# Kernel optimization log

Measured on AMD Instinct MI355X. Metric: run time of the kernel, lower is better.

## Reference

```python
import jax, jax.numpy as jnp
import numpy as np

NTYPES = 2
B, N, MNEI = 4, 512, 100
M = MNEI * NTYPES          # neighbor slots = maxNeighborNum * ntypes
EMB_LAST = 100             # embedding net sizes [25, 50, 100]
FIT_H = 240
M2 = 16
RMIN, RMAX = 0.5, 6.0


def setup_inputs():
    key = jax.random.key(0)
    ks = jax.random.split(key, 24)
    r = jax.random.uniform(ks[0], (B, N, M), minval=0.6, maxval=7.0)
    v = jax.random.normal(ks[1], (B, N, M, 3))
    v = v / jnp.linalg.norm(v, axis=-1, keepdims=True)
    keep = jax.random.uniform(ks[2], (B, N, M)) < 0.7
    ImageDR = jnp.concatenate([r[..., None], r[..., None] * v], axis=-1)
    ImageDR = jnp.where(keep[..., None], ImageDR, 0.0).astype(jnp.float32)
    Imagetype_map = jax.random.randint(ks[3], (N,), 0, NTYPES)
    list_neigh = jax.random.randint(ks[4], (B, N, M), 0, N + 1)
    type_map = jnp.arange(NTYPES)
    davg = (0.01 * jax.random.normal(ks[5], (NTYPES, M, 4))).astype(jnp.float32)
    dstd = (1.0 + 0.1 * jax.random.uniform(ks[6], (NTYPES, M, 4))).astype(jnp.float32)

    def w(k, shape, fan):
        return (jax.random.normal(k, shape) / np.sqrt(fan)).astype(jnp.float32)

    def b(k, shape):
        return (0.1 * jax.random.normal(k, shape)).astype(jnp.float32)

    emb_W0 = w(ks[7], (NTYPES, NTYPES, 1, 25), 1)
    emb_b0 = b(ks[8], (NTYPES, NTYPES, 25))
    emb_W1 = w(ks[9], (NTYPES, NTYPES, 25, 50), 25)
    emb_b1 = b(ks[10], (NTYPES, NTYPES, 50))
    emb_W2 = w(ks[11], (NTYPES, NTYPES, 50, 100), 50)
    emb_b2 = b(ks[12], (NTYPES, NTYPES, 100))
    fin = M2 * EMB_LAST
    fit_W0 = w(ks[13], (NTYPES, fin, FIT_H), fin)
    fit_b0 = b(ks[14], (NTYPES, FIT_H))
    fit_W1 = w(ks[15], (NTYPES, FIT_H, FIT_H), FIT_H)
    fit_b1 = b(ks[16], (NTYPES, FIT_H))
    fit_W2 = w(ks[17], (NTYPES, FIT_H, FIT_H), FIT_H)
    fit_b2 = b(ks[18], (NTYPES, FIT_H))
    fit_W3 = w(ks[19], (NTYPES, FIT_H, 1), FIT_H)
    fit_b3 = b(ks[20], (NTYPES, 1))
    energy_shift = jnp.array([-3.37, -5.21], dtype=jnp.float32)
    return dict(list_neigh=list_neigh, Imagetype_map=Imagetype_map, type_map=type_map,
                ImageDR=ImageDR, nghost=0, davg=davg, dstd=dstd,
                emb_W0=emb_W0, emb_b0=emb_b0, emb_W1=emb_W1, emb_b1=emb_b1,
                emb_W2=emb_W2, emb_b2=emb_b2,
                fit_W0=fit_W0, fit_b0=fit_b0, fit_W1=fit_W1, fit_b1=fit_b1,
                fit_W2=fit_W2, fit_b2=fit_b2, fit_W3=fit_W3, fit_b3=fit_b3,
                energy_shift=energy_shift)


def _emb(s, W0, b0, W1, b1, W2, b2):
    # DeepPot-SE embedding net with doubling resnet connections
    h = jnp.tanh(s @ W0 + b0)                                   # [..., 25]
    h = jnp.tanh(h @ W1 + b1) + jnp.concatenate([h, h], -1)     # [..., 50]
    return jnp.tanh(h @ W2 + b2) + jnp.concatenate([h, h], -1)  # [..., 100]


def _fit(d, W0, b0, W1, b1, W2, b2, W3, b3):
    h = jnp.tanh(d @ W0 + b0)
    h = h + jnp.tanh(h @ W1 + b1)
    h = h + jnp.tanh(h @ W2 + b2)
    return h @ W3 + b3


def _forward(ImageDR, davg, dstd,
             emb_W0, emb_b0, emb_W1, emb_b1, emb_W2, emb_b2,
             fit_W0, fit_b0, fit_W1, fit_b1, fit_W2, fit_b2, fit_W3, fit_b3,
             energy_shift, Imagetype_map):
    Bsz, Nat, Mtot, _ = ImageDR.shape
    m = Mtot // NTYPES
    R = ImageDR[..., 0]
    Rsafe = jnp.where(R > 1e-5, R, 1.0)
    # smooth switching function s(r): 1/r below Rmin, polynomial taper to Rmax
    u = (R - RMIN) / (RMAX - RMIN)
    mid = (u ** 3 * (-6.0 * u * u + 15.0 * u - 10.0) + 1.0) / Rsafe
    S = jnp.where((R > 0) & (R < RMIN), 1.0 / Rsafe,
                  jnp.where((R > RMIN) & (R < RMAX), mid, 0.0))
    msk = (jnp.abs(R) > 1e-5)[..., None]
    Ri = jnp.concatenate([S[..., None],
                          jnp.where(msk, (S / Rsafe)[..., None] * ImageDR[..., 1:4], 0.0)],
                         axis=-1)                                    # [B,N,M,4] = (s, s*x/r, s*y/r, s*z/r)
    # per-center-type normalization (irregular gather of stats)
    Rn = (Ri - davg[Imagetype_map][None]) / dstd[Imagetype_map][None]
    tmask = [(Imagetype_map == i).astype(Rn.dtype)[None, :, None, None] for i in range(NTYPES)]
    xyz = jnp.zeros((Bsz, Nat, 4, EMB_LAST), Rn.dtype)
    for j in range(NTYPES):                                          # neighbor-type slice
        sl = Rn[:, :, j * m:(j + 1) * m, :]                          # [B,N,m,4]
        s = sl[..., 0:1]
        G = jnp.zeros(sl.shape[:3] + (EMB_LAST,), sl.dtype)
        for i in range(NTYPES):                                      # center type -> pair net (i, j)
            G = G + tmask[i] * _emb(s, emb_W0[i, j], emb_b0[i, j],
                                    emb_W1[i, j], emb_b1[i, j], emb_W2[i, j], emb_b2[i, j])
        xyz = xyz + jnp.einsum('bnmk,bnmc->bnkc', sl, G)
    xyz = xyz / (m * NTYPES)
    # descriptor D = (Ri^T G)^T (Ri^T G)[:, :M2], flattened -> [B,N,EMB_LAST*M2]
    D = jnp.einsum('bnkc,bnkd->bncd', xyz, xyz[..., :M2]).reshape(Bsz, Nat, -1)
    Ei = jnp.zeros((Bsz, Nat), D.dtype)
    for i in range(NTYPES):
        e = _fit(D, fit_W0[i], fit_b0[i], fit_W1[i], fit_b1[i],
                 fit_W2[i], fit_b2[i], fit_W3[i], fit_b3[i])[..., 0] + energy_shift[i]
        Ei = Ei + tmask[i][:, :, 0, 0] * e
    Etot = jnp.sum(Ei, axis=1)
    return Etot, Ei


def reference(list_neigh, Imagetype_map, type_map, ImageDR, nghost, davg, dstd,
              emb_W0, emb_b0, emb_W1, emb_b1, emb_W2, emb_b2,
              fit_W0, fit_b0, fit_W1, fit_b1, fit_W2, fit_b2, fit_W3, fit_b3,
              energy_shift):
    return _forward(ImageDR, davg, dstd,
                    emb_W0, emb_b0, emb_W1, emb_b1, emb_W2, emb_b2,
                    fit_W0, fit_b0, fit_W1, fit_b1, fit_W2, fit_b2, fit_W3, fit_b3,
                    energy_shift, Imagetype_map)
```

## Files before the change

### kernel.cpp

```cpp
#include <hip/hip_runtime.h>
#include <math.h>

#define NT 2
#define BSZ 4
#define NAT 512
#define NATOMS 2048
#define NNEI 200
#define EMB 100
#define FITH 240
#define DDIM 1600
#define TBK 1024

#define USH_BYTE 6208
#define TBL_U   0
#define W0T_U   409600
#define W1T_U   (W0T_U + 819200)
#define W2T_U   (W1T_U + 262144)
#define D_U     (W2T_U + 262144)
#define H0_U    (D_U + 3276800)
#define USH_END (H0_U + 1048576)
#define WS_NEED ((size_t)USH_BYTE + (size_t)USH_END * 2)

typedef short s8v __attribute__((ext_vector_type(8)));
typedef float f16v __attribute__((ext_vector_type(16)));

__device__ __forceinline__ float ftanh(float x) {
    float ax = fabsf(x);
    float e = __expf(2.0f * ax);
    float t = 1.0f - __fdividef(2.0f, e + 1.0f);
    return (x < 0.0f) ? -t : t;
}
__device__ __forceinline__ unsigned short f2bf(float f) {
    unsigned u = __float_as_uint(f);
    u += 0x7FFFu + ((u >> 16) & 1u);
    return (unsigned short)(u >> 16);
}
__device__ __forceinline__ float bf2f(unsigned short s) {
    return __uint_as_float(((unsigned)s) << 16);
}
__device__ __forceinline__ float calc_S(float R) {
    float Rsafe = (R > 1e-5f) ? R : 1.0f;
    float u = (R - 0.5f) * (1.0f / 5.5f);
    float uu = u * u;
    float mid = (u * uu * (-6.0f * uu + 15.0f * u - 10.0f) + 1.0f) / Rsafe;
    float S = 0.0f;
    if (R > 0.0f && R < 0.5f)      S = 1.0f / Rsafe;
    else if (R > 0.5f && R < 6.0f) S = mid;
    return S;
}

#define N_W0 819200
#define N_W1 262144
#define N_W2 262144
#define N_B  1536
__global__ void wtrans_kernel(const float* __restrict__ fW0, const float* __restrict__ fW1,
                              const float* __restrict__ fW2,
                              const float* __restrict__ fb0, const float* __restrict__ fb1,
                              const float* __restrict__ fb2,
                              float* __restrict__ ws, float* __restrict__ out) {
    if (blockIdx.x == 0 && threadIdx.x < 4) out[threadIdx.x] = 0.0f;
    unsigned short* u0 = (unsigned short*)((char*)ws + USH_BYTE);
    int id = blockIdx.x * 256 + threadIdx.x;
    if (id < N_W0) {
        int k = id / 512, n = id - k * 512;
        float v = 0.0f;
        if (n < 240)                 v = fW0[(size_t)k * 240 + n];
        else if (n >= 256 && n < 496) v = fW0[(size_t)(1600 + k) * 240 + (n - 256)];
        u0[W0T_U + (size_t)n * 1600 + k] = f2bf(v);
        return;
    }
    id -= N_W0;
    if (id < N_W1) {
        int k = id / 512, n = id - k * 512;
        float v = 0.0f;
        if (n < 240 && k < 240)      v = fW1[(size_t)k * 240 + n];
        else if (n >= 256 && n < 496 && k >= 256 && k < 496)
                                     v = fW1[(size_t)(240 + (k - 256)) * 240 + (n - 256)];
        u0[W1T_U + (size_t)n * 512 + k] = f2bf(v);
        return;
    }
    id -= N_W1;
    if (id < N_W2) {
        int k = id / 512, n = id - k * 512;
        float v = 0.0f;
        if (n < 240 && k < 240)      v = fW2[(size_t)k * 240 + n];
        else if (n >= 256 && n < 496 && k >= 256 && k < 496)
                                     v = fW2[(size_t)(240 + (k - 256)) * 240 + (n - 256)];
        u0[W2T_U + (size_t)n * 512 + k] = f2bf(v);
        return;
    }
    id -= N_W2;
    if (id < N_B) {
        int l = id / 512, n = id - l * 512;
        const float* fb = (l == 0) ? fb0 : (l == 1) ? fb1 : fb2;
        float v = 0.0f;
        if (n < 240)                 v = fb[n];
        else if (n >= 256 && n < 496) v = fb[240 + (n - 256)];
        ws[16 + l * 512 + n] = v;
    }
}

__global__ void __launch_bounds__(256) table_kernel(
    const float* __restrict__ davg, const float* __restrict__ dstd,
    const float* __restrict__ eW0, const float* __restrict__ eb0,
    const float* __restrict__ eW1, const float* __restrict__ eb1,
    const float* __restrict__ eW2, const float* __restrict__ eb2,
    float* __restrict__ ws)
{
    __shared__ float los[100], his[100];
    __shared__ float rng[2];
    __shared__ float h0s[8][25];
    __shared__ float h1s[8][50];
    const int bx = blockIdx.x;
    const int nid = bx >> 7;
    const int kb  = (bx & 127) * 8;
    const int t = nid >> 1, j = nid & 1;
    const int tid = threadIdx.x;

    if (tid < 100) {
        int m = j * 100 + tid;
        float av = davg[(t * NNEI + m) * 4];
        float sd = dstd[(t * NNEI + m) * 4];
        float inv = __fdividef(1.0f, sd);
        float a = (0.0f - av) * inv;
        float b = (2.0f - av) * inv;
        los[tid] = fminf(a, b);
        his[tid] = fmaxf(a, b);
    }
    __syncthreads();
    if (tid == 0) {
        float lo = los[0], hi = his[0];
        for (int i = 1; i < 100; ++i) { lo = fminf(lo, los[i]); hi = fmaxf(hi, his[i]); }
        rng[0] = lo; rng[1] = hi - lo;
        if (kb == 0) {
            ws[nid * 2] = lo;
            ws[nid * 2 + 1] = (float)(TBK - 1) / (hi - lo);
        }
    }
    __syncthreads();
    const float smin = rng[0], span = rng[1];
    const float* W0 = eW0 + nid * 25;
    const float* B0 = eb0 + nid * 25;
    if (tid < 200) {
        int q = tid / 25, a = tid % 25;
        float s = smin + span * ((float)(kb + q) * (1.0f / (TBK - 1)));
        h0s[q][a] = ftanh(fmaf(s, W0[a], B0[a]));
    }
    __syncthreads();
    const float* W1 = eW1 + nid * 1250;
    const float* B1 = eb1 + nid * 50;
    for (int idx = tid; idx < 400; idx += 256) {
        int q = idx / 50, cc = idx % 50;
        float acc = B1[cc];
#pragma unroll
        for (int a = 0; a < 25; ++a) acc = fmaf(h0s[q][a], W1[a * 50 + cc], acc);
        h1s[q][cc] = ftanh(acc) + h0s[q][(cc < 25) ? cc : cc - 25];
    }
    __syncthreads();
    const float* W2 = eW2 + nid * 5000;
    const float* B2 = eb2 + nid * 100;
    unsigned short* tblu = (unsigned short*)((char*)ws + USH_BYTE) + TBL_U;
    for (int idx = tid; idx < 800; idx += 256) {
        int q = idx / 100, c = idx % 100;
        float acc = B2[c];
#pragma unroll
        for (int a = 0; a < 50; ++a) acc = fmaf(h1s[q][a], W2[a * 100 + c], acc);
        float g = ftanh(acc) + h1s[q][(c < 50) ? c : c - 50];
        tblu[(size_t)(nid * TBK + kb + q) * 100 + c] = f2bf(g);
    }
}

__global__ void __launch_bounds__(128) embed_kernel(
    const int* __restrict__ itype, const float* __restrict__ imagedr,
    const float* __restrict__ davg, const float* __restrict__ dstd,
    float* __restrict__ ws)
{
    __shared__ __align__(16) float4 srn[NNEI];
    __shared__ float sx[NNEI];
    __shared__ float part[2][400];
    const int atom = blockIdx.x;
    const int n = atom & (NAT - 1);
    const int tid = threadIdx.x;
    const int t = itype[n];
    unsigned short* u0 = (unsigned short*)((char*)ws + USH_BYTE);

    const float sm0 = ws[(t * 2 + 0) * 2], sc0 = ws[(t * 2 + 0) * 2 + 1];
    const float sm1 = ws[(t * 2 + 1) * 2], sc1 = ws[(t * 2 + 1) * 2 + 1];

    for (int m = tid; m < NNEI; m += 128) {
        float4 dr = ((const float4*)imagedr)[(size_t)atom * NNEI + m];
        float R = dr.x;
        float S = calc_S(R);
        float Rsafe = (R > 1e-5f) ? R : 1.0f;
        float sr = (fabsf(R) > 1e-5f) ? (S / Rsafe) : 0.0f;
        float4 av = ((const float4*)davg)[t * NNEI + m];
        float4 sd = ((const float4*)dstd)[t * NNEI + m];
        float4 rv;
        rv.x = (S         - av.x) / sd.x;
        rv.y = (sr * dr.y - av.y) / sd.y;
        rv.z = (sr * dr.z - av.z) / sd.z;
        rv.w = (sr * dr.w - av.w) / sd.w;
        srn[m] = rv;
        float smin = (m >= 100) ? sm1 : sm0;
        float scal = (m >= 100) ? sc1 : sc0;
        sx[m] = fminf(fmaxf((rv.x - smin) * scal, 0.0f), (float)(TBK - 2) + 0.9999f);
    }
    __syncthreads();

    const int w = tid >> 6, lane = tid & 63;
    const unsigned short* T = u0 + TBL_U + (size_t)(t * 2 + w) * TBK * EMB;
    const bool hi = (lane < 36);
    float xA0 = 0, xA1 = 0, xA2 = 0, xA3 = 0;
    float xB0 = 0, xB1 = 0, xB2 = 0, xB3 = 0;
    for (int mi = 0; mi < 100; ++mi) {
        int m = w * 100 + mi;
        float4 rv = srn[m];
        float x = sx[m];
        int i = (int)x;
        float f = x - (float)i;
        const unsigned short* Tr = T + (size_t)i * EMB;
        float g0 = bf2f(Tr[lane]);
        float g1 = bf2f(Tr[EMB + lane]);
        float g = fmaf(f, g1 - g0, g0);
        xA0 = fmaf(rv.x, g, xA0); xA1 = fmaf(rv.y, g, xA1);
        xA2 = fmaf(rv.z, g, xA2); xA3 = fmaf(rv.w, g, xA3);
        if (hi) {
            float h0v = bf2f(Tr[64 + lane]);
            float h1v = bf2f(Tr[EMB + 64 + lane]);
            float g2 = fmaf(f, h1v - h0v, h0v);
            xB0 = fmaf(rv.x, g2, xB0); xB1 = fmaf(rv.y, g2, xB1);
            xB2 = fmaf(rv.z, g2, xB2); xB3 = fmaf(rv.w, g2, xB3);
        }
    }
    part[w][0 * 100 + lane] = xA0; part[w][1 * 100 + lane] = xA1;
    part[w][2 * 100 + lane] = xA2; part[w][3 * 100 + lane] = xA3;
    if (hi) {
        part[w][0 * 100 + 64 + lane] = xB0; part[w][1 * 100 + 64 + lane] = xB1;
        part[w][2 * 100 + 64 + lane] = xB2; part[w][3 * 100 + 64 + lane] = xB3;
    }
    __syncthreads();
    const float inv = 1.0f / 200.0f;
    for (int idx = tid; idx < 400; idx += 128)
        part[0][idx] = (part[0][idx] + part[1][idx]) * inv;
    __syncthreads();
    unsigned short* Drow = u0 + D_U + (size_t)atom * DDIM;
    const float* xt = part[0];
    for (int idx = tid; idx < DDIM; idx += 128) {
        int c = idx >> 4, d = idx & 15;
        float s = xt[c] * xt[d] + xt[100 + c] * xt[100 + d]
                + xt[200 + c] * xt[200 + d] + xt[300 + c] * xt[300 + d];
        Drow[idx] = f2bf(s);
    }
}

__global__ void __launch_bounds__(256) gemm_kernel(
    const unsigned short* __restrict__ A, int lda,
    const unsigned short* __restrict__ BT, int ldb,
    const float* __restrict__ bias,
    const unsigned short* __restrict__ Res,
    unsigned short* __restrict__ Out, int ldo,
    int ksteps, int diag)
{
    __shared__ unsigned short Al[64][40];
    __shared__ unsigned short Bl[64][40];
    const int nt = blockIdx.x;
    const int mt = blockIdx.y;
    const int tid = threadIdx.x;
    const int w = tid >> 6, lane = tid & 63;
    const int wm = (w >> 1) * 32, wn = (w & 1) * 32;
    const int m0 = mt * 64, n0 = nt * 64;
    const int k_start = (diag && nt >= 4) ? 256 : 0;
    const int r4 = tid >> 2, c8 = (tid & 3) * 8;

    f16v acc;
#pragma unroll
    for (int i = 0; i < 16; ++i) acc[i] = 0.0f;

    for (int kt = 0; kt < ksteps; ++kt) {
        const int kc = k_start + kt * 32 + c8;
        uint4 av = *(const uint4*)(A  + (size_t)(m0 + r4) * lda + kc);
        uint4 bv = *(const uint4*)(BT + (size_t)(n0 + r4) * ldb + kc);
        __syncthreads();
        *(uint4*)&Al[r4][c8] = av;
        *(uint4*)&Bl[r4][c8] = bv;
        __syncthreads();
        const int fr = (lane >> 5) * 8;
        s8v a0 = *(const s8v*)&Al[wm + (lane & 31)][fr];
        s8v b0 = *(const s8v*)&Bl[wn + (lane & 31)][fr];
        acc = __builtin_amdgcn_mfma_f32_32x32x16_bf16(a0, b0, acc, 0, 0, 0);
        s8v a1 = *(const s8v*)&Al[wm + (lane & 31)][16 + fr];
        s8v b1 = *(const s8v*)&Bl[wn + (lane & 31)][16 + fr];
        acc = __builtin_amdgcn_mfma_f32_32x32x16_bf16(a1, b1, acc, 0, 0, 0);
    }

    const int gcol = n0 + wn + (lane & 31);
    const float bv = bias[gcol];
#pragma unroll
    for (int r = 0; r < 16; ++r) {
        int row = (r & 3) + 8 * (r >> 2) + 4 * (lane >> 5);
        size_t gi = (size_t)(m0 + wm + row) * ldo + gcol;
        float v = ftanh(acc[r] + bv);
        if (Res) v += bf2f(Res[gi]);
        Out[gi] = f2bf(v);
    }
}

__global__ void __launch_bounds__(256) final_kernel(
    const int* __restrict__ itype, const float* ws,
    const float* __restrict__ fW3, const float* __restrict__ fb3,
    const float* __restrict__ eshift, float* __restrict__ out)
{
    __shared__ float sred[4];
    const int tid = threadIdx.x;
    const int w = tid >> 6, lane = tid & 63;
    const int atom = blockIdx.x * 4 + w;
    const int n = atom & (NAT - 1);
    const int t = itype[n];
    const unsigned short* H = (const unsigned short*)((const char*)ws + USH_BYTE) + H0_U;
    const unsigned short* Hrow = H + (size_t)atom * 512 + t * 256;
    float p = 0.0f;
    if (lane < 60) {
        ushort4 hv = *(const ushort4*)(Hrow + lane * 4);
        const float* w3p = fW3 + t * 240 + lane * 4;
        p = bf2f(hv.x) * w3p[0] + bf2f(hv.y) * w3p[1]
          + bf2f(hv.z) * w3p[2] + bf2f(hv.w) * w3p[3];
    }
#pragma unroll
    for (int off = 32; off > 0; off >>= 1) p += __shfl_down(p, off, 64);
    if (lane == 0) {
        float e = p + fb3[t] + eshift[t];
        out[4 + atom] = e;
        sred[w] = e;
    }
    __syncthreads();
    if (tid == 0) {
        int b = (blockIdx.x * 4) >> 9;
        atomicAdd(&out[b], sred[0] + sred[1] + sred[2] + sred[3]);
    }
}

__global__ void dp_atom_kernel(
    const int* __restrict__ itype, const float* __restrict__ imagedr,
    const float* __restrict__ davg, const float* __restrict__ dstd,
    const float* __restrict__ eW0, const float* __restrict__ eb0,
    const float* __restrict__ eW1, const float* __restrict__ eb1,
    const float* __restrict__ eW2, const float* __restrict__ eb2,
    const float* __restrict__ fW0, const float* __restrict__ fb0,
    const float* __restrict__ fW1, const float* __restrict__ fb1,
    const float* __restrict__ fW2, const float* __restrict__ fb2,
    const float* __restrict__ fW3, const float* __restrict__ fb3,
    const float* __restrict__ eshift, float* __restrict__ out)
{
    __shared__ __align__(16) float4 rn4[NNEI];
    __shared__ __align__(16) float  xyz[4 * EMB];
    __shared__ __align__(16) float  h0s[100 * 25];
    __shared__ __align__(16) float  smem[100 * 52];
    const int atom = blockIdx.x;
    const int n = atom & (NAT - 1);
    const int tid = threadIdx.x;
    const int t = itype[n];
    for (int m = tid; m < NNEI; m += 256) {
        float4 dr = ((const float4*)imagedr)[(size_t)atom * NNEI + m];
        float R = dr.x;
        float S = calc_S(R);
        float Rsafe = (R > 1e-5f) ? R : 1.0f;
        float sr = (fabsf(R) > 1e-5f) ? (S / Rsafe) : 0.0f;
        float4 av = ((const float4*)davg)[t * NNEI + m];
        float4 sd = ((const float4*)dstd)[t * NNEI + m];
        float4 rv;
        rv.x = (S - av.x) / sd.x; rv.y = (sr * dr.y - av.y) / sd.y;
        rv.z = (sr * dr.z - av.z) / sd.z; rv.w = (sr * dr.w - av.w) / sd.w;
        rn4[m] = rv;
    }
    const int c = tid & 127; const int mh = tid >> 7;
    float xp0 = 0, xp1 = 0, xp2 = 0, xp3 = 0;
    for (int j = 0; j < NT; ++j) {
        const int wb = t * NT + j;
        const float* W0 = eW0 + wb * 25; const float* B0 = eb0 + wb * 25;
        const float* W1 = eW1 + wb * 1250; const float* B1 = eb1 + wb * 50;
        const float* W2 = eW2 + wb * 5000; const float* B2 = eb2 + wb * 100;
        __syncthreads();
        for (int idx = tid; idx < 2500; idx += 256) {
            int m = idx / 25, a = idx - m * 25;
            h0s[idx] = ftanh(fmaf(rn4[j * 100 + m].x, W0[a], B0[a]));
        }
        __syncthreads();
        for (int idx = tid; idx < 5000; idx += 256) {
            int m = idx / 50, cc = idx - m * 50;
            const float* h0m = h0s + m * 25;
            float acc = B1[cc];
#pragma unroll
            for (int a = 0; a < 25; ++a) acc = fmaf(h0m[a], W1[a * 50 + cc], acc);
            smem[m * 52 + cc] = ftanh(acc) + h0m[(cc < 25) ? cc : cc - 25];
        }
        for (int idx = tid; idx < 200; idx += 256)
            smem[(idx >> 1) * 52 + 50 + (idx & 1)] = 0.0f;
        __syncthreads();
        if (c < EMB) {
            float w2c[52];
#pragma unroll
            for (int a = 0; a < 50; ++a) w2c[a] = W2[a * EMB + c];
            w2c[50] = 0; w2c[51] = 0;
            const float bc = B2[c];
            const int sk = (c < 50) ? c : c - 50;
            for (int i = 0; i < 50; ++i) {
                int m = mh * 50 + i;
                const float* h1m = smem + m * 52;
                float acc = bc;
#pragma unroll
                for (int q = 0; q < 13; ++q) {
                    float4 hv = ((const float4*)h1m)[q];
                    acc = fmaf(hv.x, w2c[4 * q], acc); acc = fmaf(hv.y, w2c[4 * q + 1], acc);
                    acc = fmaf(hv.z, w2c[4 * q + 2], acc); acc = fmaf(hv.w, w2c[4 * q + 3], acc);
                }
                float g = ftanh(acc) + h1m[sk];
                float4 rm = rn4[j * 100 + m];
                xp0 = fmaf(rm.x, g, xp0); xp1 = fmaf(rm.y, g, xp1);
                xp2 = fmaf(rm.z, g, xp2); xp3 = fmaf(rm.w, g, xp3);
            }
        }
    }
    __syncthreads();
    const float inv = 1.0f / 200.0f;
    if (mh == 0 && c < EMB) {
        xyz[c] = xp0 * inv; xyz[EMB + c] = xp1 * inv;
        xyz[2 * EMB + c] = xp2 * inv; xyz[3 * EMB + c] = xp3 * inv;
    }
    __syncthreads();
    if (mh == 1 && c < EMB) {
        xyz[c] += xp0 * inv; xyz[EMB + c] += xp1 * inv;
        xyz[2 * EMB + c] += xp2 * inv; xyz[3 * EMB + c] += xp3 * inv;
    }
    __syncthreads();
    float* Dld = smem;
    for (int idx = tid; idx < DDIM; idx += 256) {
        int cc = idx >> 4, d = idx & 15;
        Dld[idx] = xyz[cc] * xyz[d] + xyz[EMB + cc] * xyz[EMB + d]
                 + xyz[2 * EMB + cc] * xyz[2 * EMB + d] + xyz[3 * EMB + cc] * xyz[3 * EMB + d];
    }
    __syncthreads();
    float* hA = smem + DDIM; float* hB = hA + FITH; float* h2 = hB + FITH; float* red = h2 + FITH;
    if (tid < FITH) {
        const float* W = fW0 + (size_t)t * DDIM * FITH;
        float acc = fb0[t * FITH + tid];
        for (int f = 0; f < DDIM; f += 4) {
            float4 dv = *(const float4*)(Dld + f);
            acc = fmaf(dv.x, W[f * FITH + tid], acc); acc = fmaf(dv.y, W[(f + 1) * FITH + tid], acc);
            acc = fmaf(dv.z, W[(f + 2) * FITH + tid], acc); acc = fmaf(dv.w, W[(f + 3) * FITH + tid], acc);
        }
        hA[tid] = ftanh(acc);
    }
    __syncthreads();
    if (tid < FITH) {
        const float* W = fW1 + t * FITH * FITH;
        float acc = fb1[t * FITH + tid];
        for (int f = 0; f < FITH; f += 4) {
            float4 hv = *(const float4*)(hA + f);
            acc = fmaf(hv.x, W[f * FITH + tid], acc); acc = fmaf(hv.y, W[(f + 1) * FITH + tid], acc);
            acc = fmaf(hv.z, W[(f + 2) * FITH + tid], acc); acc = fmaf(hv.w, W[(f + 3) * FITH + tid], acc);
        }
        hB[tid] = hA[tid] + ftanh(acc);
    }
    __syncthreads();
    if (tid < FITH) {
        const float* W = fW2 + t * FITH * FITH;
        float acc = fb2[t * FITH + tid];
        for (int f = 0; f < FITH; f += 4) {
            float4 hv = *(const float4*)(hB + f);
            acc = fmaf(hv.x, W[f * FITH + tid], acc); acc = fmaf(hv.y, W[(f + 1) * FITH + tid], acc);
            acc = fmaf(hv.z, W[(f + 2) * FITH + tid], acc); acc = fmaf(hv.w, W[(f + 3) * FITH + tid], acc);
        }
        h2[tid] = hB[tid] + ftanh(acc);
    }
    __syncthreads();
    float p = (tid < FITH) ? h2[tid] * fW3[t * FITH + tid] : 0.0f;
#pragma unroll
    for (int off = 32; off > 0; off >>= 1) p += __shfl_down(p, off, 64);
    if ((tid & 63) == 0) red[tid >> 6] = p;
    __syncthreads();
    if (tid == 0) out[4 + atom] = red[0] + red[1] + red[2] + red[3] + fb3[t] + eshift[t];
}

__global__ void etot_kernel(float* __restrict__ out) {
    const int b = blockIdx.x;
    float s = 0.0f;
    for (int n = threadIdx.x; n < NAT; n += 256) s += out[4 + b * NAT + n];
#pragma unroll
    for (int off = 32; off > 0; off >>= 1) s += __shfl_down(s, off, 64);
    __shared__ float rr[4];
    if ((threadIdx.x & 63) == 0) rr[threadIdx.x >> 6] = s;
    __syncthreads();
    if (threadIdx.x == 0) out[b] = rr[0] + rr[1] + rr[2] + rr[3];
}

extern "C" void kernel_launch(void* const* d_in, const int* in_sizes, int n_in,
                              void* d_out, int out_size, void* d_ws, size_t ws_size,
                              hipStream_t stream) {
    const int*   itype   = (const int*)  d_in[1];
    const float* imagedr = (const float*)d_in[3];
    const float* davg    = (const float*)d_in[5];
    const float* dstd    = (const float*)d_in[6];
    const float* eW0     = (const float*)d_in[7];
    const float* eb0     = (const float*)d_in[8];
    const float* eW1     = (const float*)d_in[9];
    const float* eb1     = (const float*)d_in[10];
    const float* eW2     = (const float*)d_in[11];
    const float* eb2     = (const float*)d_in[12];
    const float* fW0     = (const float*)d_in[13];
    const float* fb0     = (const float*)d_in[14];
    const float* fW1     = (const float*)d_in[15];
    const float* fb1     = (const float*)d_in[16];
    const float* fW2     = (const float*)d_in[17];
    const float* fb2     = (const float*)d_in[18];
    const float* fW3     = (const float*)d_in[19];
    const float* fb3     = (const float*)d_in[20];
    const float* eshift  = (const float*)d_in[21];
    float* out = (float*)d_out;
    float* ws  = (float*)d_ws;

    if (ws_size >= WS_NEED) {
        unsigned short* u0 = (unsigned short*)((char*)ws + USH_BYTE);
        const int n_wt = (N_W0 + N_W1 + N_W2 + N_B + 255) / 256;
        wtrans_kernel<<<n_wt, 256, 0, stream>>>(fW0, fW1, fW2, fb0, fb1, fb2, ws, out);
        table_kernel<<<512, 256, 0, stream>>>(davg, dstd, eW0, eb0, eW1, eb1, eW2, eb2, ws);
        embed_kernel<<<NATOMS, 128, 0, stream>>>(itype, imagedr, davg, dstd, ws);
        gemm_kernel<<<dim3(8, 32), 256, 0, stream>>>(
            u0 + D_U, DDIM, u0 + W0T_U, DDIM, ws + 16, nullptr, u0 + H0_U, 512, 50, 0);
        gemm_kernel<<<dim3(8, 32), 256, 0, stream>>>(
            u0 + H0_U, 512, u0 + W1T_U, 512, ws + 16 + 512, u0 + H0_U, u0 + D_U, 512, 8, 1);
        gemm_kernel<<<dim3(8, 32), 256, 0, stream>>>(
            u0 + D_U, 512, u0 + W2T_U, 512, ws + 16 + 1024, u0 + D_U, u0 + H0_U, 512, 8, 1);
        final_kernel<<<512, 256, 0, stream>>>(itype, ws, fW3, fb3, eshift, out);
    } else {
        dp_atom_kernel<<<NATOMS, 256, 0, stream>>>(itype, imagedr, davg, dstd,
            eW0, eb0, eW1, eb1, eW2, eb2,
            fW0, fb0, fW1, fb1, fW2, fb2, fW3, fb3, eshift, out);
        etot_kernel<<<BSZ, 256, 0, stream>>>(out);
    }
}
```

Before: 194.7 us.

## Replace LDS-tiled GEMM with small-tile MFMA GEMM and fuse final projection

The 64x64 LDS-staged GEMM using 32x32 MFMA is replaced by a one-wave kernel that computes 16x32 tiles with 16x16x32 bf16 MFMA, reading operands straight from global memory. This gives many more blocks and removes the LDS barriers. The last fitting layer now folds the W3 dot product into its epilogue with shuffles and atomic adds into per-atom energies, which the weight-transpose kernel pre-seeds with bias plus energy shift. The separate final kernel is dropped and a plain etot reduction is used instead. The weight transpose now writes coalesced, and the embed loop is unrolled by two. The costs are the loss of LDS reuse, so each tile rereads global memory, and the nondeterministic ordering of the float atomics.

```diff
diff --git a/kernel.cpp b/kernel.cpp
--- a/kernel.cpp
+++ b/kernel.cpp
@@ -11,18 +11,21 @@
 #define DDIM 1600
 #define TBK 1024
 
-#define USH_BYTE 6208
+#define BIAS_F  16
+#define W3C_F   (BIAS_F + 3 * 512)
+#define USH_BYTE 8320
 #define TBL_U   0
 #define W0T_U   409600
 #define W1T_U   (W0T_U + 819200)
 #define W2T_U   (W1T_U + 262144)
 #define D_U     (W2T_U + 262144)
 #define H0_U    (D_U + 3276800)
-#define USH_END (H0_U + 1048576)
+#define H1_U    (H0_U + 1048576)
+#define USH_END (H1_U + 1048576)
 #define WS_NEED ((size_t)USH_BYTE + (size_t)USH_END * 2)
 
 typedef short s8v __attribute__((ext_vector_type(8)));
-typedef float f16v __attribute__((ext_vector_type(16)));
+typedef float f4v __attribute__((ext_vector_type(4)));
 
 __device__ __forceinline__ float ftanh(float x) {
     float ax = fabsf(x);
@@ -53,40 +56,43 @@
 #define N_W1 262144
 #define N_W2 262144
 #define N_B  1536
+#define N_W3 512
+#define N_EI 2048
 __global__ void wtrans_kernel(const float* __restrict__ fW0, const float* __restrict__ fW1,
                               const float* __restrict__ fW2,
                               const float* __restrict__ fb0, const float* __restrict__ fb1,
                               const float* __restrict__ fb2,
+                              const float* __restrict__ fW3, const float* __restrict__ fb3,
+                              const float* __restrict__ eshift, const int* __restrict__ itype,
                               float* __restrict__ ws, float* __restrict__ out) {
-    if (blockIdx.x == 0 && threadIdx.x < 4) out[threadIdx.x] = 0.0f;
     unsigned short* u0 = (unsigned short*)((char*)ws + USH_BYTE);
     int id = blockIdx.x * 256 + threadIdx.x;
     if (id < N_W0) {
-        int k = id / 512, n = id - k * 512;
+        int n = id / 1600, k = id - n * 1600;
         float v = 0.0f;
-        if (n < 240)                 v = fW0[(size_t)k * 240 + n];
+        if (n < 240)                  v = fW0[(size_t)k * 240 + n];
         else if (n >= 256 && n < 496) v = fW0[(size_t)(1600 + k) * 240 + (n - 256)];
-        u0[W0T_U + (size_t)n * 1600 + k] = f2bf(v);
+        u0[W0T_U + id] = f2bf(v);
         return;
     }
     id -= N_W0;
     if (id < N_W1) {
-        int k = id / 512, n = id - k * 512;
+        int n = id / 512, k = id - n * 512;
         float v = 0.0f;
-        if (n < 240 && k < 240)      v = fW1[(size_t)k * 240 + n];
+        if (n < 240 && k < 240)       v = fW1[(size_t)k * 240 + n];
         else if (n >= 256 && n < 496 && k >= 256 && k < 496)
-                                     v = fW1[(size_t)(240 + (k - 256)) * 240 + (n - 256)];
-        u0[W1T_U + (size_t)n * 512 + k] = f2bf(v);
+                                      v = fW1[(size_t)(240 + (k - 256)) * 240 + (n - 256)];
+        u0[W1T_U + id] = f2bf(v);
         return;
     }
     id -= N_W1;
     if (id < N_W2) {
-        int k = id / 512, n = id - k * 512;
+        int n = id / 512, k = id - n * 512;
         float v = 0.0f;
-        if (n < 240 && k < 240)      v = fW2[(size_t)k * 240 + n];
+        if (n < 240 && k < 240)       v = fW2[(size_t)k * 240 + n];
         else if (n >= 256 && n < 496 && k >= 256 && k < 496)
-                                     v = fW2[(size_t)(240 + (k - 256)) * 240 + (n - 256)];
-        u0[W2T_U + (size_t)n * 512 + k] = f2bf(v);
+                                      v = fW2[(size_t)(240 + (k - 256)) * 240 + (n - 256)];
+        u0[W2T_U + id] = f2bf(v);
         return;
     }
     id -= N_W2;
@@ -94,9 +100,24 @@
         int l = id / 512, n = id - l * 512;
         const float* fb = (l == 0) ? fb0 : (l == 1) ? fb1 : fb2;
         float v = 0.0f;
-        if (n < 240)                 v = fb[n];
+        if (n < 240)                  v = fb[n];
         else if (n >= 256 && n < 496) v = fb[240 + (n - 256)];
-        ws[16 + l * 512 + n] = v;
+        ws[BIAS_F + l * 512 + n] = v;
+        return;
+    }
+    id -= N_B;
+    if (id < N_W3) {
+        int n = id;
+        float v = 0.0f;
+        if (n < 240)                  v = fW3[n];
+        else if (n >= 256 && n < 496) v = fW3[240 + (n - 256)];
+        ws[W3C_F + n] = v;
+        return;
+    }
+    id -= N_W3;
+    if (id < N_EI) {
+        int t = itype[id & (NAT - 1)];
+        out[4 + id] = fb3[t] + eshift[t];
     }
 }
 
@@ -212,6 +233,7 @@
     const bool hi = (lane < 36);
     float xA0 = 0, xA1 = 0, xA2 = 0, xA3 = 0;
     float xB0 = 0, xB1 = 0, xB2 = 0, xB3 = 0;
+#pragma unroll 2
     for (int mi = 0; mi < 100; ++mi) {
         int m = w * 100 + mi;
         float4 rv = srn[m];
@@ -253,90 +275,82 @@
     }
 }
 
-__global__ void __launch_bounds__(256) gemm_kernel(
+__global__ void __launch_bounds__(64) gemm16_kernel(
     const unsigned short* __restrict__ A, int lda,
     const unsigned short* __restrict__ BT, int ldb,
     const float* __restrict__ bias,
     const unsigned short* __restrict__ Res,
     unsigned short* __restrict__ Out, int ldo,
-    int ksteps, int diag)
+    const float* __restrict__ w3c, const int* __restrict__ itype,
+    float* __restrict__ out,
+    int ksteps, int diag, int mode)
 {
-    __shared__ unsigned short Al[64][40];
-    __shared__ unsigned short Bl[64][40];
-    const int nt = blockIdx.x;
-    const int mt = blockIdx.y;
-    const int tid = threadIdx.x;
-    const int w = tid >> 6, lane = tid & 63;
-    const int wm = (w >> 1) * 32, wn = (w & 1) * 32;
-    const int m0 = mt * 64, n0 = nt * 64;
-    const int k_start = (diag && nt >= 4) ? 256 : 0;
-    const int r4 = tid >> 2, c8 = (tid & 3) * 8;
-
-    f16v acc;
-#pragma unroll
-    for (int i = 0; i < 16; ++i) acc[i] = 0.0f;
-
+    const int lane = threadIdx.x;
+    const int bx = blockIdx.x;
+    const int by = blockIdx.y;
+    const int m0 = by * 16, n0 = bx * 32;
+    const int k0 = (diag && bx >= 8) ? 256 : 0;
+    const int mr = lane & 15;
+    const int q  = lane >> 4;
+    const unsigned short* Ap  = A  + (size_t)(m0 + mr) * lda + k0 + q * 8;
+    const unsigned short* B0p = BT + (size_t)(n0 + mr) * ldb + k0 + q * 8;
+    const unsigned short* B1p = B0p + (size_t)16 * ldb;
+
+    f4v acc0 = {0.0f, 0.0f, 0.0f, 0.0f};
+    f4v acc1 = {0.0f, 0.0f, 0.0f, 0.0f};
+#pragma unroll 2
     for (int kt = 0; kt < ksteps; ++kt) {
-        const int kc = k_start + kt * 32 + c8;
-        uint4 av = *(const uint4*)(A  + (size_t)(m0 + r4) * lda + kc);
-        uint4 bv = *(const uint4*)(BT + (size_t)(n0 + r4) * ldb + kc);
-        __syncthreads();
-        *(uint4*)&Al[r4][c8] = av;
-        *(uint4*)&Bl[r4][c8] = bv;
-        __syncthreads();
-        const int fr = (lane >> 5) * 8;
-        s8v a0 = *(const s8v*)&Al[wm + (lane & 31)][fr];
-        s8v b0 = *(const s8v*)&Bl[wn + (lane & 31)][fr];
-        acc = __builtin_amdgcn_mfma_f32_32x32x16_bf16(a0, b0, acc, 0, 0, 0);
-        s8v a1 = *(const s8v*)&Al[wm + (lane & 31)][16 + fr];
-        s8v b1 = *(const s8v*)&Bl[wn + (lane & 31)][16 + fr];
-        acc = __builtin_amdgcn_mfma_f32_32x32x16_bf16(a1, b1, acc, 0, 0, 0);
-    }
-
-    const int gcol = n0 + wn + (lane & 31);
-    const float bv = bias[gcol];
-#pragma unroll
-    for (int r = 0; r < 16; ++r) {
-        int row = (r & 3) + 8 * (r >> 2) + 4 * (lane >> 5);
-        size_t gi = (size_t)(m0 + wm + row) * ldo + gcol;
-        float v = ftanh(acc[r] + bv);
-        if (Res) v += bf2f(Res[gi]);
-        Out[gi] = f2bf(v);
-    }
-}
-
-__global__ void __launch_bounds__(256) final_kernel(
-    const int* __restrict__ itype, const float* ws,
-    const float* __restrict__ fW3, const float* __restrict__ fb3,
-    const float* __restrict__ eshift, float* __restrict__ out)
-{
-    __shared__ float sred[4];
-    const int tid = threadIdx.x;
-    const int w = tid >> 6, lane = tid & 63;
-    const int atom = blockIdx.x * 4 + w;
-    const int n = atom & (NAT - 1);
-    const int t = itype[n];
-    const unsigned short* H = (const unsigned short*)((const char*)ws + USH_BYTE) + H0_U;
-    const unsigned short* Hrow = H + (size_t)atom * 512 + t * 256;
-    float p = 0.0f;
-    if (lane < 60) {
-        ushort4 hv = *(const ushort4*)(Hrow + lane * 4);
-        const float* w3p = fW3 + t * 240 + lane * 4;
-        p = bf2f(hv.x) * w3p[0] + bf2f(hv.y) * w3p[1]
-          + bf2f(hv.z) * w3p[2] + bf2f(hv.w) * w3p[3];
-    }
-#pragma unroll
-    for (int off = 32; off > 0; off >>= 1) p += __shfl_down(p, off, 64);
-    if (lane == 0) {
-        float e = p + fb3[t] + eshift[t];
-        out[4 + atom] = e;
-        sred[w] = e;
-    }
-    __syncthreads();
-    if (tid == 0) {
-        int b = (blockIdx.x * 4) >> 9;
-        atomicAdd(&out[b], sred[0] + sred[1] + sred[2] + sred[3]);
-    }
+        s8v av = *(const s8v*)(Ap  + kt * 32);
+        s8v b0 = *(const s8v*)(B0p + kt * 32);
+        s8v b1 = *(const s8v*)(B1p + kt * 32);
+        acc0 = __builtin_amdgcn_mfma_f32_16x16x32_bf16(av, b0, acc0, 0, 0, 0);
+        acc1 = __builtin_amdgcn_mfma_f32_16x16x32_bf16(av, b1, acc1, 0, 0, 0);
+    }
+
+    const int g0 = n0 + mr, g1 = n0 + 16 + mr;
+    const float bv0 = bias[g0], bv1 = bias[g1];
+    if (mode < 2) {
+#pragma unroll
+        for (int r = 0; r < 4; ++r) {
+            int row = m0 + q * 4 + r;
+            size_t i0 = (size_t)row * ldo + g0;
+            size_t i1 = (size_t)row * ldo + g1;
+            float v0 = ftanh(acc0[r] + bv0);
+            float v1 = ftanh(acc1[r] + bv1);
+            if (mode == 1) { v0 += bf2f(Res[i0]); v1 += bf2f(Res[i1]); }
+            Out[i0] = f2bf(v0); Out[i1] = f2bf(v1);
+        }
+    } else {
+        const int seg = (bx >= 8);
+        const float w30 = w3c[g0], w31 = w3c[g1];
+#pragma unroll
+        for (int r = 0; r < 4; ++r) {
+            int row = m0 + q * 4 + r;
+            size_t i0 = (size_t)row * ldo + g0;
+            size_t i1 = (size_t)row * ldo + g1;
+            float v0 = bf2f(Res[i0]) + ftanh(acc0[r] + bv0);
+            float v1 = bf2f(Res[i1]) + ftanh(acc1[r] + bv1);
+            float p = v0 * w30 + v1 * w31;
+            p += __shfl_xor(p, 1, 16);
+            p += __shfl_xor(p, 2, 16);
+            p += __shfl_xor(p, 4, 16);
+            p += __shfl_xor(p, 8, 16);
+            if (mr == 0 && itype[row & (NAT - 1)] == seg)
+                atomicAdd(&out[4 + row], p);
+        }
+    }
+}
+
+__global__ void etot_kernel(float* __restrict__ out) {
+    const int b = blockIdx.x;
+    float s = 0.0f;
+    for (int n = threadIdx.x; n < NAT; n += 256) s += out[4 + b * NAT + n];
+#pragma unroll
+    for (int off = 32; off > 0; off >>= 1) s += __shfl_down(s, off, 64);
+    __shared__ float rr[4];
+    if ((threadIdx.x & 63) == 0) rr[threadIdx.x >> 6] = s;
+    __syncthreads();
+    if (threadIdx.x == 0) out[b] = rr[0] + rr[1] + rr[2] + rr[3];
 }
 
 __global__ void dp_atom_kernel(
@@ -481,18 +495,6 @@
     if (tid == 0) out[4 + atom] = red[0] + red[1] + red[2] + red[3] + fb3[t] + eshift[t];
 }
 
-__global__ void etot_kernel(float* __restrict__ out) {
-    const int b = blockIdx.x;
-    float s = 0.0f;
-    for (int n = threadIdx.x; n < NAT; n += 256) s += out[4 + b * NAT + n];
-#pragma unroll
-    for (int off = 32; off > 0; off >>= 1) s += __shfl_down(s, off, 64);
-    __shared__ float rr[4];
-    if ((threadIdx.x & 63) == 0) rr[threadIdx.x >> 6] = s;
-    __syncthreads();
-    if (threadIdx.x == 0) out[b] = rr[0] + rr[1] + rr[2] + rr[3];
-}
-
 extern "C" void kernel_launch(void* const* d_in, const int* in_sizes, int n_in,
                               void* d_out, int out_size, void* d_ws, size_t ws_size,
                               hipStream_t stream) {
@@ -520,17 +522,21 @@
 
     if (ws_size >= WS_NEED) {
         unsigned short* u0 = (unsigned short*)((char*)ws + USH_BYTE);
-        const int n_wt = (N_W0 + N_W1 + N_W2 + N_B + 255) / 256;
-        wtrans_kernel<<<n_wt, 256, 0, stream>>>(fW0, fW1, fW2, fb0, fb1, fb2, ws, out);
+        const int n_ids = N_W0 + N_W1 + N_W2 + N_B + N_W3 + N_EI;
+        wtrans_kernel<<<(n_ids + 255) / 256, 256, 0, stream>>>(
+            fW0, fW1, fW2, fb0, fb1, fb2, fW3, fb3, eshift, itype, ws, out);
         table_kernel<<<512, 256, 0, stream>>>(davg, dstd, eW0, eb0, eW1, eb1, eW2, eb2, ws);
         embed_kernel<<<NATOMS, 128, 0, stream>>>(itype, imagedr, davg, dstd, ws);
-        gemm_kernel<<<dim3(8, 32), 256, 0, stream>>>(
-            u0 + D_U, DDIM, u0 + W0T_U, DDIM, ws + 16, nullptr, u0 + H0_U, 512, 50, 0);
-        gemm_kernel<<<dim3(8, 32), 256, 0, stream>>>(
-            u0 + H0_U, 512, u0 + W1T_U, 512, ws + 16 + 512, u0 + H0_U, u0 + D_U, 512, 8, 1);
-        gemm_kernel<<<dim3(8, 32), 256, 0, stream>>>(
-            u0 + D_U, 512, u0 + W2T_U, 512, ws + 16 + 1024, u0 + D_U, u0 + H0_U, 512, 8, 1);
-        final_kernel<<<512, 256, 0, stream>>>(itype, ws, fW3, fb3, eshift, out);
+        gemm16_kernel<<<dim3(16, 128), 64, 0, stream>>>(
+            u0 + D_U, DDIM, u0 + W0T_U, DDIM, ws + BIAS_F,
+            nullptr, u0 + H0_U, 512, nullptr, nullptr, nullptr, 50, 0, 0);
+        gemm16_kernel<<<dim3(16, 128), 64, 0, stream>>>(
+            u0 + H0_U, 512, u0 + W1T_U, 512, ws + BIAS_F + 512,
+            u0 + H0_U, u0 + H1_U, 512, nullptr, nullptr, nullptr, 8, 1, 0 + 1);
+        gemm16_kernel<<<dim3(16, 128), 64, 0, stream>>>(
+            u0 + H1_U, 512, u0 + W2T_U, 512, ws + BIAS_F + 1024,
+            u0 + H1_U, nullptr, 512, ws + W3C_F, itype, out, 8, 1, 2);
+        etot_kernel<<<BSZ, 256, 0, stream>>>(out);
     } else {
         dp_atom_kernel<<<NATOMS, 256, 0, stream>>>(itype, imagedr, davg, dstd,
             eW0, eb0, eW1, eb1, eW2, eb2,
```

New measurement: 202.9 us. 1.04x slower.
